# Performance work log

Measured on AMD Instinct MI355X. Metric: run time of the kernel, lower is better.

The kernel has to match this reference:

```python
import jax, jax.numpy as jnp
import numpy as np

B, N, D, K, C = 8, 4096, 128, 16, 64  # batch, points, in_channels, knn, growth_rate


def _knn_idx(pos, k):
    # pos: (B, N, 3); returns (B, N, k) nearest-neighbor indices excluding self (offset=1)
    sq = jnp.sum(pos * pos, axis=-1)  # (B, N)
    d2 = sq[:, :, None] + sq[:, None, :] - 2.0 * jnp.einsum('bnd,bmd->bnm', pos, pos)
    _, idx = jax.lax.top_k(-d2, k + 1)  # sorted ascending by distance
    return idx[:, :, 1:]


def _knn_group(x, idx):
    # x: (B, N, F), idx: (B, N, K) -> (B, N, K, F)
    return jax.vmap(lambda xb, ib: xb[ib])(x, idx)


def setup_inputs():
    key = jax.random.key(0)
    ks = jax.random.split(key, 10)
    sc = 0.05
    return {
        'x': jax.random.normal(ks[0], (B, N, D), jnp.float32),
        'pos': jax.random.normal(ks[1], (B, N, 3), jnp.float32),
        'W_first': jax.random.normal(ks[2], (3 * D, C), jnp.float32) * sc,
        'b_first': jnp.zeros((C,), jnp.float32),
        'W_mid1': jax.random.normal(ks[3], (D + C, C), jnp.float32) * sc,
        'b_mid1': jnp.zeros((C,), jnp.float32),
        'W_mid2': jax.random.normal(ks[4], (D + 2 * C, C), jnp.float32) * sc,
        'b_mid2': jnp.zeros((C,), jnp.float32),
        'W_last': jax.random.normal(ks[5], (D + 3 * C, C), jnp.float32) * sc,
        'b_last': jnp.zeros((C,), jnp.float32),
    }


def reference(x, pos, W_first, b_first, W_mid1, b_mid1, W_mid2, b_mid2, W_last, b_last):
    knn_idx = _knn_idx(pos, K)                      # (B, N, K)
    knn_feat = _knn_group(x, knn_idx)               # (B, N, K, D)
    x_tiled = jnp.broadcast_to(x[:, :, None, :], knn_feat.shape)
    edge_feat = jnp.concatenate([x_tiled, knn_feat, knn_feat - x_tiled], axis=-1)  # (B,N,K,3D)

    y = jnp.concatenate([jax.nn.relu(edge_feat @ W_first + b_first), x_tiled], axis=-1)  # (B,N,K,D+C)
    y = jnp.concatenate([jax.nn.relu(y @ W_mid1 + b_mid1), y], axis=-1)                  # (B,N,K,D+2C)
    y = jnp.concatenate([jax.nn.relu(y @ W_mid2 + b_mid2), y], axis=-1)                  # (B,N,K,D+3C)
    y = jnp.concatenate([y @ W_last + b_last, y], axis=-1)                               # (B,N,K,D+4C)
    return jnp.max(y, axis=2)                       # (B, N, D+4C)
```

## Files before the change

kernel.cpp:

```cpp
#include <hip/hip_runtime.h>
#include <hip/hip_bf16.h>

typedef unsigned int uint;
typedef unsigned short ushort_t;
typedef unsigned long long u64;
typedef __attribute__((ext_vector_type(2))) unsigned long long u64x2;
typedef __attribute__((ext_vector_type(8))) short short8;
typedef __attribute__((ext_vector_type(4))) float floatx4;

#define NB 8
#define NP 4096
#define ND 128
#define NK 16
#define NC 64
#define NPTS 32768
#define QB 8
#define CAP5 256
#define NQE 8

__device__ __forceinline__ float bf2f(ushort_t h){ return __uint_as_float(((uint)h)<<16); }
__device__ __forceinline__ ushort_t f2bf(float f){
  uint u = __float_as_uint(f);
  u = u + 0x7FFFu + ((u>>16)&1u);
  return (ushort_t)(u>>16);
}
__device__ __forceinline__ float ldin(const void* p, long i, int f32){
  return f32 ? ((const float*)p)[i] : bf2f(((const ushort_t*)p)[i]);
}
__device__ __forceinline__ void stout(void* o, long i, float v, int f32){
  if (f32) ((float*)o)[i] = v; else ((ushort_t*)o)[i] = f2bf(v);
}

#define SWZE(row, e) (((row)<<6) + ((e) ^ (((row)&7)<<3)))
#define WAVE_SYNC() asm volatile("s_waitcnt lgkmcnt(0)" ::: "memory")

__global__ __launch_bounds__(256) void k_prep(const void* __restrict__ pos, float4* __restrict__ posf,
                        const void* __restrict__ Wf, const void* __restrict__ bfv,
                        const void* __restrict__ Wm1, const void* __restrict__ bm1,
                        const void* __restrict__ Wm2, const void* __restrict__ bm2,
                        const void* __restrict__ Wl, const void* __restrict__ bl,
                        ushort_t* __restrict__ WcatT, float* __restrict__ biasT,
                        ushort_t* __restrict__ Wtiles, int* __restrict__ flag){
#pragma clang fp contract(off)
  __shared__ int cnt;
  if (threadIdx.x == 0) cnt = 0;
  __syncthreads();
  {
    const uint* w = (const uint*)Wf;
    int c = 0;
    for (int i = threadIdx.x; i < 512; i += 256){
      uint u = w[i];
      uint e = (u >> 7) & 0xFFu;
      c += (e >= 100u && e < 128u) ? 1 : 0;
    }
    atomicAdd(&cnt, c);
  }
  __syncthreads();
  int f32 = (cnt < 256) ? 1 : 0;
  if (blockIdx.x == 0 && threadIdx.x == 0) *flag = f32;

  if (blockIdx.x < 128){
    int p = blockIdx.x*256 + threadIdx.x;
    float x = ldin(pos, (long)p*3+0, f32);
    float y = ldin(pos, (long)p*3+1, f32);
    float z = ldin(pos, (long)p*3+2, f32);
    float px = x*x; float py = y*y; float pz = z*z;
    float sq = (px + py) + pz;
    posf[p] = make_float4(-2.0f*x, -2.0f*y, -2.0f*z, sq);
    return;
  }
  int id = (blockIdx.x - 128)*256 + threadIdx.x;
  if (id < 40960){
    int n = id >> 7, k = id & 127;
    float v;
    if (n < 64)       v = ldin(Wf, (long)k*64 + n, f32) - ldin(Wf, (long)(256+k)*64 + n, f32);
    else if (n < 128) v = ldin(Wf, (long)(128+k)*64 + (n-64), f32) + ldin(Wf, (long)(256+k)*64 + (n-64), f32);
    else if (n < 192) v = ldin(Wm1, (long)(64+k)*64 + (n-128), f32);
    else if (n < 256) v = ldin(Wm2, (long)(128+k)*64 + (n-192), f32);
    else              v = ldin(Wl, (long)(192+k)*64 + (n-256), f32);
    WcatT[id] = f2bf(v);
  } else if (id < 41280){
    int n = id - 40960;
    float bv;
    if (n < 64)       bv = ldin(bfv, n, f32);
    else if (n < 128) bv = 0.0f;
    else if (n < 192) bv = ldin(bm1, n-128, f32);
    else if (n < 256) bv = ldin(bm2, n-192, f32);
    else              bv = ldin(bl, n-256, f32);
    biasT[n] = bv;
  } else if (id < 65856){
    int t2 = id - 41280;
    int tile = t2 >> 10;
    int r    = (t2 >> 6) & 15;
    int ep   = t2 & 63;
    int kl   = ep ^ ((r & 7) << 3);
    float v;
    if (tile < 4){
      int n = tile*16 + r;
      v = ldin(Wm1, (long)kl*64 + n, f32);
    } else if (tile < 12){
      int u = tile - 4; int n = (u >> 1)*16 + r; int k = (u & 1)*64 + kl;
      v = ldin(Wm2, (long)k*64 + n, f32);
    } else {
      int u = tile - 12; int n = (u / 3)*16 + r; int k = (u % 3)*64 + kl;
      v = ldin(Wl, (long)k*64 + n, f32);
    }
    Wtiles[t2] = f2bf(v);
  }
}

__global__ __launch_bounds__(256) void k_knn(const float4* __restrict__ posf, int* __restrict__ knn){
#pragma clang fp contract(off)
  __shared__ ushort_t sjl[QB][CAP5];
  __shared__ __align__(16) u64 kw[4][CAP5];
  __shared__ int scnt[QB];
  __shared__ uint sut[QB];
  int tid = threadIdx.x;
  int lane = tid & 63;
  int wave = tid >> 6;
  int qbase = blockIdx.x * QB;
  int jbase = (qbase >> 12) << 12;
  if (tid < QB){ scnt[tid] = 0; sut[tid] = 0xFFFFFFFFu; }
  __syncthreads();
  float4 Qr[QB];
  #pragma unroll
  for (int q = 0; q < QB; ++q){
    float4 q2 = posf[qbase + q];
    Qr[q] = make_float4(-0.5f*q2.x, -0.5f*q2.y, -0.5f*q2.z, q2.w);
  }
  float lmg[QB];
  #pragma unroll
  for (int q = 0; q < QB; ++q) lmg[q] = 3.0e38f;
  for (int s = 0; s < 16; ++s){
    float4 p2 = posf[jbase + s*256 + tid];
    #pragma unroll
    for (int q = 0; q < QB; ++q){
      float g = __builtin_fmaf(Qr[q].x, p2.x, __builtin_fmaf(Qr[q].y, p2.y,
                __builtin_fmaf(Qr[q].z, p2.z, p2.w)));
      lmg[q] = fminf(lmg[q], g);
    }
  }
  uint lmb[QB];
  #pragma unroll
  for (int q = 0; q < QB; ++q)
    lmb[q] = __float_as_uint(fmaxf(lmg[q] + Qr[q].w, 0.0f));
  int lo[QB], hi[QB];
  #pragma unroll
  for (int q = 0; q < QB; ++q){ lo[q] = 0; hi[q] = 4095; }
  for (int it = 0; it < 12; ++it){
    #pragma unroll
    for (int q = 0; q < QB; ++q){
      int mid = (lo[q] + hi[q]) >> 1;
      uint T = (uint)(mid+1) << 19;
      u64 bal = __ballot(lmb[q] < T);
      bool c = __popcll(bal) >= 17;
      hi[q] = c ? mid : hi[q];
      lo[q] = c ? lo[q] : mid + 1;
    }
  }
  #pragma unroll
  for (int q = 0; q < QB; ++q){
    if (lane == 0) atomicMin(&sut[q], (uint)(lo[q]+2) << 19);
  }
  __syncthreads();
  float Tc[QB];
  #pragma unroll
  for (int q = 0; q < QB; ++q){
    float Tf = __uint_as_float(sut[q]);
    float S  = (Qr[q].w + 16.0f) * 6.103515625e-05f;
    Tc[q] = (Tf + S) - Qr[q].w;
  }
  for (int s = 0; s < 16; ++s){
    int j = s*256 + tid;
    float4 p2 = posf[jbase + j];
    #pragma unroll
    for (int q = 0; q < QB; ++q){
      float g = __builtin_fmaf(Qr[q].x, p2.x, __builtin_fmaf(Qr[q].y, p2.y,
                __builtin_fmaf(Qr[q].z, p2.z, p2.w)));
      if (g < Tc[q]){
        int pc = atomicAdd(&scnt[q], 1);
        if (pc < CAP5) sjl[q][pc] = (ushort_t)j;
      }
    }
  }
  __syncthreads();
  for (int q = wave; q < QB; q += 4){
    int cnt = scnt[q]; if (cnt > CAP5) cnt = CAP5;
    float4 Qq2 = posf[qbase + q];
    float qx = -0.5f*Qq2.x, qy = -0.5f*Qq2.y, qz = -0.5f*Qq2.z, qw = Qq2.w;
    for (int base = 0; base < cnt; base += 64){
      int ci = base + lane;
      if (ci < cnt){
        int j = sjl[q][ci];
        float4 p2 = posf[jbase + j];
        float px = -0.5f*p2.x, py = -0.5f*p2.y, pz = -0.5f*p2.z;
        float ax = qx*px; float ay = qy*py; float az = qz*pz;
        float dot = (ax + ay) + az;
        float t  = qw + p2.w;
        float v  = t - 2.0f*dot;
        uint w = __float_as_uint(v);
        uint sd = w ^ ((w & 0x80000000u) ? 0xFFFFFFFFu : 0x80000000u);
        kw[wave][ci] = (((u64)sd) << 32) | (uint)j;
      }
    }
    WAVE_SYNC();
    const u64* kwp = kw[wave];
    for (int base = 0; base < cnt; base += 64){
      int ci = base + lane;
      u64 mykey = (ci < cnt) ? kwp[ci] : ~0ull;
      int r = 0;
      int i = 0;
      #pragma unroll 2
      for (; i + 1 < cnt; i += 2){
        u64x2 two = *(const u64x2*)&kwp[i];
        r += (two[0] < mykey) ? 1 : 0;
        r += (two[1] < mykey) ? 1 : 0;
      }
      if (i < cnt) r += (kwp[i] < mykey) ? 1 : 0;
      if (ci < cnt && r >= 1 && r <= 16)
        knn[(qbase + q)*16 + (r-1)] = (int)(mykey & 0xFFFFFFFFu);
    }
    WAVE_SYNC();
  }
}

__global__ __launch_bounds__(256) void k_pgemm(const void* __restrict__ xv, const ushort_t* __restrict__ WcatT,
                                               const float* __restrict__ biasT, ushort_t* __restrict__ P,
                                               const int* __restrict__ flag){
  int f32 = *flag;
  int wave = threadIdx.x >> 6, lane = threadIdx.x & 63;
  int rowbase = blockIdx.x*64 + wave*16;
  int quad = lane >> 4, col = lane & 15;
  floatx4 acc[20];
  #pragma unroll
  for (int i = 0; i < 20; ++i) acc[i] = (floatx4){0.f,0.f,0.f,0.f};
  #pragma unroll
  for (int kk = 0; kk < 4; ++kk){
    int k = kk*32 + quad*8;
    short8 a;
    if (f32){
      const float* xf = (const float*)xv + (long)(rowbase + col)*128 + k;
      #pragma unroll
      for (int i = 0; i < 8; ++i) a[i] = (short)f2bf(xf[i]);
    } else {
      a = *(const short8*)((const ushort_t*)xv + (long)(rowbase + col)*128 + k);
    }
    #pragma unroll
    for (int nt = 0; nt < 20; ++nt){
      short8 bb = *(const short8*)(WcatT + (nt*16 + col)*128 + k);
      acc[nt] = __builtin_amdgcn_mfma_f32_16x16x32_bf16(a, bb, acc[nt], 0, 0, 0);
    }
  }
  #pragma unroll
  for (int nt = 0; nt < 20; ++nt){
    float bv = biasT[nt*16 + col];
    #pragma unroll
    for (int r = 0; r < 4; ++r){
      int m = quad*4 + r;
      P[(long)(rowbase + m)*320 + nt*16 + col] = f2bf(acc[nt][r] + bv);
    }
  }
}

__global__ __launch_bounds__(512) void k_edge(const void* __restrict__ x, const ushort_t* __restrict__ P,
                                              const int* __restrict__ knn,
                                              const ushort_t* __restrict__ Wg, void* __restrict__ out,
                                              const int* __restrict__ flag){
  __shared__ __align__(16) ushort_t wlds[12*1024];
  __shared__ __align__(16) ushort_t hb[8][3][1024];
  int f32 = *flag;
  int tid = threadIdx.x;
  int wave = tid >> 6, lane = tid & 63;
  int quad = lane >> 4, col = lane & 15;
  int lb = ((blockIdx.x & 7) << 6) | (blockIdx.x >> 3);
  int qid0 = lb*(8*NQE) + wave*NQE;
  int b = qid0 >> 12;
  const ushort_t* Pb = P + ((long)(b<<12))*320;
  int e4 = lane >> 2, cg = lane & 3;

  int idxv[NQE];
  #pragma unroll
  for (int iq = 0; iq < NQE; ++iq)
    idxv[iq] = knn[(qid0+iq)*16 + e4] & (NP - 1);
  short8 nk0 = *(const short8*)(Pb + (long)idxv[0]*320 + 64 + cg*16);
  short8 nk1 = *(const short8*)(Pb + (long)idxv[0]*320 + 64 + cg*16 + 8);
  short8 nq0 = *(const short8*)(P + (long)qid0*320 + cg*16);
  short8 nq1 = *(const short8*)(P + (long)qid0*320 + cg*16 + 8);

  #pragma unroll
  for (int i = 0; i < 3; ++i){
    int e = (i*512 + tid) << 3;
    *(short8*)(wlds + e) = *(const short8*)(Wg + e);
  }
  __syncthreads();
  const ushort_t* wA  = wlds;
  const ushort_t* wB  = wlds + 4*1024;
  const ushort_t* wCg = Wg + 12*1024;
  ushort_t* h1p = hb[wave][0];
  ushort_t* h2p = hb[wave][1];
  ushort_t* h3p = hb[wave][2];

  #pragma unroll
  for (int iq = 0; iq < NQE; ++iq){
    int qid = qid0 + iq;
    const ushort_t* Prow = P + (long)qid*320;
    long outb = (long)qid*384;

    float u1v[4], u2v[4], u3v[4];
    #pragma unroll
    for (int nt = 0; nt < 4; ++nt){
      u1v[nt] = bf2f(Prow[128 + nt*16 + col]);
      u2v[nt] = bf2f(Prow[192 + nt*16 + col]);
      u3v[nt] = bf2f(Prow[256 + nt*16 + col]);
    }

    short8 k0 = nk0, k1 = nk1, q0 = nq0, q1 = nq1;
    if (iq + 1 < NQE){
      nk0 = *(const short8*)(Pb + (long)idxv[iq+1]*320 + 64 + cg*16);
      nk1 = *(const short8*)(Pb + (long)idxv[iq+1]*320 + 64 + cg*16 + 8);
      nq0 = *(const short8*)(P + (long)(qid+1)*320 + cg*16);
      nq1 = *(const short8*)(P + (long)(qid+1)*320 + cg*16 + 8);
    }

    {
      short8 h0, h1r;
      #pragma unroll
      for (int i = 0; i < 8; ++i){
        float v = fmaxf(bf2f((ushort_t)q0[i]) + bf2f((ushort_t)k0[i]), 0.0f);
        h0[i] = (short)f2bf(v);
        float w = fmaxf(bf2f((ushort_t)q1[i]) + bf2f((ushort_t)k1[i]), 0.0f);
        h1r[i] = (short)f2bf(w);
      }
      *(short8*)(h1p + SWZE(e4, cg*16))     = h0;
      *(short8*)(h1p + SWZE(e4, cg*16 + 8)) = h1r;
    }
    WAVE_SYNC();

    floatx4 acc2[4];
    #pragma unroll
    for (int nt = 0; nt < 4; ++nt) acc2[nt] = (floatx4){0.f,0.f,0.f,0.f};
    #pragma unroll
    for (int kk = 0; kk < 2; ++kk){
      int k = kk*32 + quad*8;
      short8 a = *(const short8*)(h1p + SWZE(col, k));
      #pragma unroll
      for (int nt = 0; nt < 4; ++nt){
        short8 bb = *(const short8*)(wA + nt*1024 + SWZE(col, k));
        acc2[nt] = __builtin_amdgcn_mfma_f32_16x16x32_bf16(a, bb, acc2[nt], 0, 0, 0);
      }
    }
    #pragma unroll
    for (int nt = 0; nt < 4; ++nt){
      float v0 = fmaxf(acc2[nt][0] + u1v[nt], 0.0f);
      float v1 = fmaxf(acc2[nt][1] + u1v[nt], 0.0f);
      float v2 = fmaxf(acc2[nt][2] + u1v[nt], 0.0f);
      float v3 = fmaxf(acc2[nt][3] + u1v[nt], 0.0f);
      h2p[SWZE(quad*4+0, nt*16+col)] = f2bf(v0);
      h2p[SWZE(quad*4+1, nt*16+col)] = f2bf(v1);
      h2p[SWZE(quad*4+2, nt*16+col)] = f2bf(v2);
      h2p[SWZE(quad*4+3, nt*16+col)] = f2bf(v3);
      float m2 = fmaxf(fmaxf(v0, v1), fmaxf(v2, v3));
      m2 = fmaxf(m2, __shfl_xor(m2, 16, 64));
      m2 = fmaxf(m2, __shfl_xor(m2, 32, 64));
      if (lane < 16) stout(out, outb + 128 + nt*16 + lane, bf2f(f2bf(m2)), f32);
    }
    WAVE_SYNC();

    floatx4 acc3[4];
    #pragma unroll
    for (int nt = 0; nt < 4; ++nt) acc3[nt] = (floatx4){0.f,0.f,0.f,0.f};
    #pragma unroll
    for (int kk = 0; kk < 4; ++kk){
      int kg = kk*32 + quad*8;
      const ushort_t* src = (kk < 2) ? h2p : h1p;
      int kl = (kk < 2) ? kg : (kg - 64);
      short8 a = *(const short8*)(src + SWZE(col, kl));
      #pragma unroll
      for (int nt = 0; nt < 4; ++nt){
        short8 bb = *(const short8*)(wB + (nt*2 + (kg>>6))*1024 + SWZE(col, kg & 63));
        acc3[nt] = __builtin_amdgcn_mfma_f32_16x16x32_bf16(a, bb, acc3[nt], 0, 0, 0);
      }
    }
    #pragma unroll
    for (int nt = 0; nt < 4; ++nt){
      float v0 = fmaxf(acc3[nt][0] + u2v[nt], 0.0f);
      float v1 = fmaxf(acc3[nt][1] + u2v[nt], 0.0f);
      float v2 = fmaxf(acc3[nt][2] + u2v[nt], 0.0f);
      float v3 = fmaxf(acc3[nt][3] + u2v[nt], 0.0f);
      h3p[SWZE(quad*4+0, nt*16+col)] = f2bf(v0);
      h3p[SWZE(quad*4+1, nt*16+col)] = f2bf(v1);
      h3p[SWZE(quad*4+2, nt*16+col)] = f2bf(v2);
      h3p[SWZE(quad*4+3, nt*16+col)] = f2bf(v3);
      float m3 = fmaxf(fmaxf(v0, v1), fmaxf(v2, v3));
      m3 = fmaxf(m3, __shfl_xor(m3, 16, 64));
      m3 = fmaxf(m3, __shfl_xor(m3, 32, 64));
      if (lane < 16) stout(out, outb + 64 + nt*16 + lane, bf2f(f2bf(m3)), f32);
    }
    WAVE_SYNC();

    floatx4 acc4[4];
    #pragma unroll
    for (int nt = 0; nt < 4; ++nt) acc4[nt] = (floatx4){0.f,0.f,0.f,0.f};
    #pragma unroll
    for (int kk = 0; kk < 6; ++kk){
      int kg = kk*32 + quad*8;
      const ushort_t* src = (kk < 2) ? h3p : ((kk < 4) ? h2p : h1p);
      int kl = (kk < 2) ? kg : ((kk < 4) ? (kg - 64) : (kg - 128));
      short8 a = *(const short8*)(src + SWZE(col, kl));
      #pragma unroll
      for (int nt = 0; nt < 4; ++nt){
        short8 bb = *(const short8*)(wCg + (nt*3 + (kg>>6))*1024 + SWZE(col, kg & 63));
        acc4[nt] = __builtin_amdgcn_mfma_f32_16x16x32_bf16(a, bb, acc4[nt], 0, 0, 0);
      }
    }
    #pragma unroll
    for (int nt = 0; nt < 4; ++nt){
      float m0 = fmaxf(fmaxf(acc4[nt][0], acc4[nt][1]), fmaxf(acc4[nt][2], acc4[nt][3])) + u3v[nt];
      m0 = fmaxf(m0, __shfl_xor(m0, 16, 64));
      m0 = fmaxf(m0, __shfl_xor(m0, 32, 64));
      if (lane < 16) stout(out, outb + nt*16 + lane, m0, f32);
    }
    {
      ushort_t mx1 = 0;
      #pragma unroll
      for (int m = 0; m < 16; ++m){
        ushort_t v1u = h1p[SWZE(m, lane)]; if (v1u > mx1) mx1 = v1u;
      }
      stout(out, outb + 192 + lane, bf2f(mx1), f32);
      stout(out, outb + 256 + lane,      ldin(x, (long)qid*128 + lane, f32), f32);
      stout(out, outb + 256 + 64 + lane, ldin(x, (long)qid*128 + 64 + lane, f32), f32);
    }
    WAVE_SYNC();
  }
}

extern "C" void kernel_launch(void* const* d_in, const int* in_sizes, int n_in,
                              void* d_out, int out_size, void* d_ws, size_t ws_size,
                              hipStream_t stream){
  const void* x   = d_in[0];
  const void* pos = d_in[1];
  const void* Wf  = d_in[2];
  const void* bfv = d_in[3];
  const void* Wm1 = d_in[4];
  const void* bm1 = d_in[5];
  const void* Wm2 = d_in[6];
  const void* bm2 = d_in[7];
  const void* Wl  = d_in[8];
  const void* bl  = d_in[9];
  char* ws = (char*)d_ws;
  float4*   posf   = (float4*)(ws + 0);
  int*      knn    = (int*)(ws + 524288);
  ushort_t* P      = (ushort_t*)(ws + 2621440);
  ushort_t* WcatT  = (ushort_t*)(ws + 23592960);
  float*    biasT  = (float*)(ws + 23674880);
  ushort_t* Wtiles = (ushort_t*)(ws + 23676160);
  int*      flag   = (int*)(ws + 23725312);

  k_prep <<<386,   256, 0, stream>>>(pos, posf, Wf, bfv, Wm1, bm1, Wm2, bm2, Wl, bl,
                                     WcatT, biasT, Wtiles, flag);
  k_knn  <<<4096,  256, 0, stream>>>(posf, knn);
  k_pgemm<<<512,   256, 0, stream>>>(x, WcatT, biasT, P, flag);
  k_edge <<<512,   512, 0, stream>>>(x, P, knn, Wtiles, d_out, flag);
}
```

Baseline: 289.5 us.

## Build first-layer edge features directly in MFMA A-operand registers, skip LDS staging

Each lane now loads the query and neighbor projections in the MFMA A-fragment layout and computes the first hidden layer in registers, so the LDS write, wave sync and re-reads of h1 are removed. The first weight block is read from global memory instead of LDS, which shrinks LDS use and may allow more blocks per CU. The h1 max over neighbors uses packed bf16 shuffle reductions instead of 16 LDS reads. The tradeoff is more shuffles and global weight loads that now rely on cache hits, plus the query feature is reloaded per query rather than prefetched.

```diff
diff --git a/kernel.cpp b/kernel.cpp
--- a/kernel.cpp
+++ b/kernel.cpp
@@ -7,6 +7,7 @@
 typedef __attribute__((ext_vector_type(2))) unsigned long long u64x2;
 typedef __attribute__((ext_vector_type(8))) short short8;
 typedef __attribute__((ext_vector_type(4))) float floatx4;
+typedef __attribute__((ext_vector_type(4))) uint uintx4;
 
 #define NB 8
 #define NP 4096
@@ -29,6 +30,13 @@
 }
 __device__ __forceinline__ void stout(void* o, long i, float v, int f32){
   if (f32) ((float*)o)[i] = v; else ((ushort_t*)o)[i] = f2bf(v);
+}
+__device__ __forceinline__ uint umax2(uint a, uint b){
+  uint al = a & 0xFFFFu, bl = b & 0xFFFFu;
+  uint ah = a >> 16,     bh = b >> 16;
+  uint lo = (al > bl) ? al : bl;
+  uint hi = (ah > bh) ? ah : bh;
+  return (hi << 16) | lo;
 }
 
 #define SWZE(row, e) (((row)<<6) + ((e) ^ (((row)&7)<<3)))
@@ -266,8 +274,8 @@
                                               const int* __restrict__ knn,
                                               const ushort_t* __restrict__ Wg, void* __restrict__ out,
                                               const int* __restrict__ flag){
-  __shared__ __align__(16) ushort_t wlds[12*1024];
-  __shared__ __align__(16) ushort_t hb[8][3][1024];
+  __shared__ __align__(16) ushort_t wlds[8*1024];
+  __shared__ __align__(16) ushort_t hb[8][2][1024];
   int f32 = *flag;
   int tid = threadIdx.x;
   int wave = tid >> 6, lane = tid & 63;
@@ -276,29 +284,25 @@
   int qid0 = lb*(8*NQE) + wave*NQE;
   int b = qid0 >> 12;
   const ushort_t* Pb = P + ((long)(b<<12))*320;
-  int e4 = lane >> 2, cg = lane & 3;
 
   int idxv[NQE];
   #pragma unroll
   for (int iq = 0; iq < NQE; ++iq)
-    idxv[iq] = knn[(qid0+iq)*16 + e4] & (NP - 1);
-  short8 nk0 = *(const short8*)(Pb + (long)idxv[0]*320 + 64 + cg*16);
-  short8 nk1 = *(const short8*)(Pb + (long)idxv[0]*320 + 64 + cg*16 + 8);
-  short8 nq0 = *(const short8*)(P + (long)qid0*320 + cg*16);
-  short8 nq1 = *(const short8*)(P + (long)qid0*320 + cg*16 + 8);
-
-  #pragma unroll
-  for (int i = 0; i < 3; ++i){
+    idxv[iq] = knn[(qid0+iq)*16 + col] & (NP - 1);
+  short8 nkf0 = *(const short8*)(Pb + (long)idxv[0]*320 + 64 + quad*8);
+  short8 nkf1 = *(const short8*)(Pb + (long)idxv[0]*320 + 96 + quad*8);
+
+  #pragma unroll
+  for (int i = 0; i < 2; ++i){
     int e = (i*512 + tid) << 3;
-    *(short8*)(wlds + e) = *(const short8*)(Wg + e);
-  }
-  __syncthreads();
-  const ushort_t* wA  = wlds;
-  const ushort_t* wB  = wlds + 4*1024;
+    *(short8*)(wlds + e) = *(const short8*)(Wg + 4*1024 + e);
+  }
+  __syncthreads();
+  const ushort_t* wAg = Wg;
+  const ushort_t* wB  = wlds;
   const ushort_t* wCg = Wg + 12*1024;
-  ushort_t* h1p = hb[wave][0];
-  ushort_t* h2p = hb[wave][1];
-  ushort_t* h3p = hb[wave][2];
+  ushort_t* h2p = hb[wave][0];
+  ushort_t* h3p = hb[wave][1];
 
   #pragma unroll
   for (int iq = 0; iq < NQE; ++iq){
@@ -313,28 +317,21 @@
       u2v[nt] = bf2f(Prow[192 + nt*16 + col]);
       u3v[nt] = bf2f(Prow[256 + nt*16 + col]);
     }
-
-    short8 k0 = nk0, k1 = nk1, q0 = nq0, q1 = nq1;
+    short8 qa0 = *(const short8*)(Prow + quad*8);
+    short8 qa1 = *(const short8*)(Prow + 32 + quad*8);
+
+    short8 k0 = nkf0, k1 = nkf1;
     if (iq + 1 < NQE){
-      nk0 = *(const short8*)(Pb + (long)idxv[iq+1]*320 + 64 + cg*16);
-      nk1 = *(const short8*)(Pb + (long)idxv[iq+1]*320 + 64 + cg*16 + 8);
-      nq0 = *(const short8*)(P + (long)(qid+1)*320 + cg*16);
-      nq1 = *(const short8*)(P + (long)(qid+1)*320 + cg*16 + 8);
-    }
-
-    {
-      short8 h0, h1r;
-      #pragma unroll
-      for (int i = 0; i < 8; ++i){
-        float v = fmaxf(bf2f((ushort_t)q0[i]) + bf2f((ushort_t)k0[i]), 0.0f);
-        h0[i] = (short)f2bf(v);
-        float w = fmaxf(bf2f((ushort_t)q1[i]) + bf2f((ushort_t)k1[i]), 0.0f);
-        h1r[i] = (short)f2bf(w);
-      }
-      *(short8*)(h1p + SWZE(e4, cg*16))     = h0;
-      *(short8*)(h1p + SWZE(e4, cg*16 + 8)) = h1r;
-    }
-    WAVE_SYNC();
+      nkf0 = *(const short8*)(Pb + (long)idxv[iq+1]*320 + 64 + quad*8);
+      nkf1 = *(const short8*)(Pb + (long)idxv[iq+1]*320 + 96 + quad*8);
+    }
+
+    short8 f0, f1;
+    #pragma unroll
+    for (int i = 0; i < 8; ++i){
+      f0[i] = (short)f2bf(fmaxf(bf2f((ushort_t)qa0[i]) + bf2f((ushort_t)k0[i]), 0.0f));
+      f1[i] = (short)f2bf(fmaxf(bf2f((ushort_t)qa1[i]) + bf2f((ushort_t)k1[i]), 0.0f));
+    }
 
     floatx4 acc2[4];
     #pragma unroll
@@ -342,10 +339,10 @@
     #pragma unroll
     for (int kk = 0; kk < 2; ++kk){
       int k = kk*32 + quad*8;
-      short8 a = *(const short8*)(h1p + SWZE(col, k));
+      short8 a = (kk == 0) ? f0 : f1;
       #pragma unroll
       for (int nt = 0; nt < 4; ++nt){
-        short8 bb = *(const short8*)(wA + nt*1024 + SWZE(col, k));
+        short8 bb = *(const short8*)(wAg + nt*1024 + SWZE(col, k));
         acc2[nt] = __builtin_amdgcn_mfma_f32_16x16x32_bf16(a, bb, acc2[nt], 0, 0, 0);
       }
     }
@@ -372,9 +369,9 @@
     #pragma unroll
     for (int kk = 0; kk < 4; ++kk){
       int kg = kk*32 + quad*8;
-      const ushort_t* src = (kk < 2) ? h2p : h1p;
-      int kl = (kk < 2) ? kg : (kg - 64);
-      short8 a = *(const short8*)(src + SWZE(col, kl));
+      short8 a;
+      if (kk < 2)      a = *(const short8*)(h2p + SWZE(col, kg));
+      else             a = (kk == 2) ? f0 : f1;
       #pragma unroll
       for (int nt = 0; nt < 4; ++nt){
         short8 bb = *(const short8*)(wB + (nt*2 + (kg>>6))*1024 + SWZE(col, kg & 63));
@@ -404,9 +401,10 @@
     #pragma unroll
     for (int kk = 0; kk < 6; ++kk){
       int kg = kk*32 + quad*8;
-      const ushort_t* src = (kk < 2) ? h3p : ((kk < 4) ? h2p : h1p);
-      int kl = (kk < 2) ? kg : ((kk < 4) ? (kg - 64) : (kg - 128));
-      short8 a = *(const short8*)(src + SWZE(col, kl));
+      short8 a;
+      if (kk < 2)      a = *(const short8*)(h3p + SWZE(col, kg));
+      else if (kk < 4) a = *(const short8*)(h2p + SWZE(col, kg - 64));
+      else             a = (kk == 4) ? f0 : f1;
       #pragma unroll
       for (int nt = 0; nt < 4; ++nt){
         short8 bb = *(const short8*)(wCg + (nt*3 + (kg>>6))*1024 + SWZE(col, kg & 63));
@@ -421,12 +419,27 @@
       if (lane < 16) stout(out, outb + nt*16 + lane, m0, f32);
     }
     {
-      ushort_t mx1 = 0;
+      uintx4 w0 = *(uintx4*)&f0;
+      uintx4 w1 = *(uintx4*)&f1;
       #pragma unroll
-      for (int m = 0; m < 16; ++m){
-        ushort_t v1u = h1p[SWZE(m, lane)]; if (v1u > mx1) mx1 = v1u;
-      }
-      stout(out, outb + 192 + lane, bf2f(mx1), f32);
+      for (int m = 1; m <= 8; m <<= 1){
+        #pragma unroll
+        for (int j = 0; j < 4; ++j){
+          uint o0 = (uint)__shfl_xor((int)w0[j], m, 64);
+          uint o1 = (uint)__shfl_xor((int)w1[j], m, 64);
+          w0[j] = umax2(w0[j], o0);
+          w1[j] = umax2(w1[j], o1);
+        }
+      }
+      if (col == 0){
+        #pragma unroll
+        for (int j = 0; j < 4; ++j){
+          stout(out, outb + 192 + quad*8 + 2*j,          bf2f((ushort_t)(w0[j] & 0xFFFFu)), f32);
+          stout(out, outb + 192 + quad*8 + 2*j + 1,      bf2f((ushort_t)(w0[j] >> 16)), f32);
+          stout(out, outb + 192 + 32 + quad*8 + 2*j,     bf2f((ushort_t)(w1[j] & 0xFFFFu)), f32);
+          stout(out, outb + 192 + 32 + quad*8 + 2*j + 1, bf2f((ushort_t)(w1[j] >> 16)), f32);
+        }
+      }
       stout(out, outb + 256 + lane,      ldin(x, (long)qid*128 + lane, f32), f32);
       stout(out, outb + 256 + 64 + lane, ldin(x, (long)qid*128 + 64 + lane, f32), f32);
     }
```

Measured after the change: 325.8 us. +12.5%, slower.
